# Kernel tuning notes

Measured on AMD Instinct MI355X. Metric: run time of the kernel, lower is better.

## Reference

```python
import jax, jax.numpy as jnp
import numpy as np

B, T, D, MP = 32, 256, 512, 20


def setup_inputs() -> dict:
    key = jax.random.key(0)
    k1, k2, k3 = jax.random.split(key, 3)
    reps_lt = jax.random.normal(k1, (B, T, D), dtype=jnp.float32)
    reps_rt = jax.random.normal(k2, (B, T, D), dtype=jnp.float32)
    kernel = jax.random.normal(k3, (1, 1, 1, MP, D), dtype=jnp.float32)
    return {"reps_lt": reps_lt, "reps_rt": reps_rt, "kernel": kernel}


def reference(reps_lt, reps_rt, kernel):
    # kernel: (1,1,1,m,d) -> (m,d)
    km = kernel.reshape(kernel.shape[-2], kernel.shape[-1])
    # scores[b,t,s,m] = sum_d lt[b,t,d] * km[m,d] * rt[b,s,d]
    # matches original broadcast-multiply + sum over d (cosine_norm=False path)
    scores = jnp.einsum('btd,md,bsd->btsm', reps_lt, km, reps_rt)
    match = jnp.tanh(scores)               # [b, t1, t2, m]
    return jnp.max(match, axis=2)          # max-pool over t2 -> [b, t1, m]
```

## Files before the change

### kernel.cpp

```cpp
#include <hip/hip_runtime.h>


constexpr int TT = 256;
constexpr int DD = 512;
constexpr int NM = 20;
constexpr int NB = 32;
constexpr int BM = 128;
constexpr int BK = 32;
constexpr int NK = DD / BK;

typedef short bf16x8 __attribute__((ext_vector_type(8)));
typedef float f32x4  __attribute__((ext_vector_type(4)));

__device__ __forceinline__ void async_ld16(const void* g, void* l) {
    __builtin_amdgcn_global_load_lds(
        (const __attribute__((address_space(1))) void*)g,
        (__attribute__((address_space(3))) void*)l, 16, 0, 0);
}

__device__ __forceinline__ unsigned pack_bf16(float lo, float hi) {
    unsigned ulo = __builtin_bit_cast(unsigned, lo);
    unsigned uhi = __builtin_bit_cast(unsigned, hi);
    return (ulo >> 16) | (uhi & 0xFFFF0000u);
}

__device__ __forceinline__ unsigned mulpack(unsigned a2, float k0, float k1) {
    float f0 = __builtin_bit_cast(float, a2 << 16) * k0;
    float f1 = __builtin_bit_cast(float, a2 & 0xFFFF0000u) * k1;
    return __builtin_amdgcn_perm(__builtin_bit_cast(unsigned, f1),
                                 __builtin_bit_cast(unsigned, f0), 0x07060302u);
}

__global__ __launch_bounds__(256)
void cast_bf16(const float* __restrict__ lt, const float* __restrict__ rt,
               unsigned short* __restrict__ ltb, unsigned short* __restrict__ rtb)
{
    const int half = (int)gridDim.x >> 1;
    int bid = blockIdx.x;
    const float* src;
    unsigned short* dst;
    if (bid < half) { src = lt; dst = ltb; }
    else            { src = rt; dst = rtb; bid -= half; }
    size_t base = ((size_t)bid * 256 + threadIdx.x) * 8;
    float4 a = *(const float4*)(src + base);
    float4 b = *(const float4*)(src + base + 4);
    uint4 w;
    w.x = pack_bf16(a.x, a.y);
    w.y = pack_bf16(a.z, a.w);
    w.z = pack_bf16(b.x, b.y);
    w.w = pack_bf16(b.z, b.w);
    *(uint4*)(dst + base) = w;
}

__global__ __launch_bounds__(256, 4)
void mp_match_split(const unsigned short* __restrict__ ltb, const unsigned short* __restrict__ rtb,
                    const float* __restrict__ km, float* __restrict__ part)
{
    __shared__ __attribute__((aligned(16))) unsigned short Ash[2][BM * 4 * 8];
    __shared__ __attribute__((aligned(16))) unsigned short Bsh[2][BM * 4 * 8];
    __shared__ __attribute__((aligned(16))) float kmf[DD];
    __shared__ __attribute__((aligned(16))) float maxbuf[2][BM];

    const int f  = blockIdx.x;
    const int c8 = f & 7;
    const int i  = f >> 3;
    const int b  = c8 + 8 * (i / 80);
    const int j  = i % 80;
    const int m  = j >> 2;
    const int t0 = ((j >> 1) & 1) * 128;
    const int s0 = (j & 1) * 128;
    const int sT = j & 1;

    const int tid  = threadIdx.x;
    const int w    = tid >> 6;
    const int lane = tid & 63;
    const int l15  = lane & 15;
    const int l4   = lane >> 4;
    const int wt   = (w & 1) * 64;
    const int wsO  = (w >> 1) * 64;

    kmf[tid]       = km[(size_t)m * DD + tid];
    kmf[tid + 256] = km[(size_t)m * DD + tid + 256];

    const unsigned short* ltB = ltb + ((size_t)b * TT + t0) * DD;
    const unsigned short* rtB = rtb + ((size_t)b * TT + s0) * DD;

    const int ar0 = tid >> 2,        ac = tid & 3;
    const int ar1 = (tid + 256) >> 2;
    const int ap0 = ac ^ ((ar0 >> 1) & 3);
    const int ap1 = ac ^ ((ar1 >> 1) & 3);
    const unsigned short* aSrc0 = ltB + (size_t)ar0 * DD + ac * 8;
    const unsigned short* aSrc1 = ltB + (size_t)ar1 * DD + ac * 8;

    auto issueB = [&](int kk, int buf) {
        const int kb = kk * BK;
#pragma unroll
        for (int q = 0; q < 2; ++q) {
            int slot = q * 256 + tid;
            int row = slot >> 2;
            int c = (slot & 3) ^ ((slot >> 3) & 3);
            async_ld16(rtB + (size_t)row * DD + kb + c * 8,
                       (char*)&Bsh[buf][0] + (size_t)slot * 16);
        }
    };
    auto aload = [&](int kk, uint4* ar) {
        ar[0] = *(const uint4*)(aSrc0 + kk * BK);
        ar[1] = *(const uint4*)(aSrc1 + kk * BK);
    };
    auto scaleWrite = [&](int kk, int buf, const uint4* ar) {
        float4 k0 = *(const float4*)&kmf[kk * BK + ac * 8];
        float4 k1 = *(const float4*)&kmf[kk * BK + ac * 8 + 4];
        uint4 o;
        o.x = mulpack(ar[0].x, k0.x, k0.y);
        o.y = mulpack(ar[0].y, k0.z, k0.w);
        o.z = mulpack(ar[0].z, k1.x, k1.y);
        o.w = mulpack(ar[0].w, k1.z, k1.w);
        *(uint4*)&Ash[buf][(size_t)(ar0 * 4 + ap0) * 8] = o;
        o.x = mulpack(ar[1].x, k0.x, k0.y);
        o.y = mulpack(ar[1].y, k0.z, k0.w);
        o.z = mulpack(ar[1].z, k1.x, k1.y);
        o.w = mulpack(ar[1].w, k1.z, k1.w);
        *(uint4*)&Ash[buf][(size_t)(ar1 * 4 + ap1) * 8] = o;
    };

    f32x4 acc[4][4] = {};
    uint4 ar[2];

    aload(0, ar);
    issueB(0, 0);
    __syncthreads();
    scaleWrite(0, 0, ar);

    const int fpos = l4 ^ ((l15 >> 1) & 3);

    for (int kk = 0; kk < NK; ++kk) {
        const int buf = kk & 1;
        __syncthreads();
        if (kk + 1 < NK) {
            aload(kk + 1, ar);
            issueB(kk + 1, buf ^ 1);
        }
        bf16x8 af[4], bv[4];
#pragma unroll
        for (int ii = 0; ii < 4; ++ii)
            af[ii] = *(const bf16x8*)&Ash[buf][(size_t)((wt + ii * 16 + l15) * 4 + fpos) * 8];
#pragma unroll
        for (int jj = 0; jj < 4; ++jj)
            bv[jj] = *(const bf16x8*)&Bsh[buf][(size_t)((wsO + jj * 16 + l15) * 4 + fpos) * 8];
#pragma unroll
        for (int ii = 0; ii < 4; ++ii)
#pragma unroll
            for (int jj = 0; jj < 4; ++jj)
                acc[ii][jj] = __builtin_amdgcn_mfma_f32_16x16x32_bf16(af[ii], bv[jj], acc[ii][jj], 0, 0, 0);
        if (kk + 1 < NK)
            scaleWrite(kk + 1, buf ^ 1, ar);
    }

#pragma unroll
    for (int ii = 0; ii < 4; ++ii) {
        f32x4 v = acc[ii][0];
#pragma unroll
        for (int jj = 1; jj < 4; ++jj) {
            v.x = fmaxf(v.x, acc[ii][jj].x);
            v.y = fmaxf(v.y, acc[ii][jj].y);
            v.z = fmaxf(v.z, acc[ii][jj].z);
            v.w = fmaxf(v.w, acc[ii][jj].w);
        }
#pragma unroll
        for (int off = 1; off < 16; off <<= 1) {
            v.x = fmaxf(v.x, __shfl_xor(v.x, off, 64));
            v.y = fmaxf(v.y, __shfl_xor(v.y, off, 64));
            v.z = fmaxf(v.z, __shfl_xor(v.z, off, 64));
            v.w = fmaxf(v.w, __shfl_xor(v.w, off, 64));
        }
        if (l15 == 0)
            *(f32x4*)&maxbuf[w >> 1][wt + ii * 16 + l4 * 4] = v;
    }
    __syncthreads();
    if (tid < BM) {
        float v = fmaxf(maxbuf[0][tid], maxbuf[1][tid]);
        part[(((size_t)sT * NB + b) * TT + t0 + tid) * NM + m] = v;
    }
}

__global__ __launch_bounds__(256)
void mp_combine(const float* __restrict__ part, float* __restrict__ out, int n)
{
    int idx = blockIdx.x * 256 + threadIdx.x;
    if (idx < n)
        out[idx] = tanhf(fmaxf(part[idx], part[(size_t)n + idx]));
}

__global__ __launch_bounds__(256, 2)
void mp_match_kernel(const float* __restrict__ lt, const float* __restrict__ rt,
                     const float* __restrict__ km, float* __restrict__ out)
{
    __shared__ __attribute__((aligned(16))) unsigned short Ash[2][4][128][8];
    __shared__ __attribute__((aligned(16))) unsigned short Bsh2[2][4][256][8];
    __shared__ __attribute__((aligned(16))) float maxbuf[2][128];

    const int ttile = blockIdx.x, m = blockIdx.y, b = blockIdx.z;
    const int t0 = ttile * 128;
    const int tid = threadIdx.x, wave = tid >> 6, lane = tid & 63;
    const int l15 = lane & 15, l4 = lane >> 4;
    const int wt = (wave & 1) * 64, wsi = wave >> 1;

    const float* ltp = lt + ((size_t)b * TT + t0) * DD;
    const float* rtp = rt + (size_t)b * TT * DD;
    const float* kmp = km + (size_t)m * DD;
    const int a_t = tid >> 1, a_h = tid & 1;

    f32x4 acc[4][8] = {};

    auto stage = [&](int kk, int buf) {
        const int d0 = kk * BK;
        const float* ap = ltp + (size_t)a_t * DD + d0 + a_h * 16;
        const float* kp = kmp + d0 + a_h * 16;
#pragma unroll
        for (int q = 0; q < 2; ++q) {
            float4 x0 = *(const float4*)(ap + q * 8);
            float4 x1 = *(const float4*)(ap + q * 8 + 4);
            float4 k0 = *(const float4*)(kp + q * 8);
            float4 k1 = *(const float4*)(kp + q * 8 + 4);
            uint4 wv;
            wv.x = pack_bf16(x0.x * k0.x, x0.y * k0.y);
            wv.y = pack_bf16(x0.z * k0.z, x0.w * k0.w);
            wv.z = pack_bf16(x1.x * k1.x, x1.y * k1.y);
            wv.w = pack_bf16(x1.z * k1.z, x1.w * k1.w);
            *(uint4*)&Ash[buf][a_h * 2 + q][a_t][0] = wv;
        }
        const float* bp = rtp + (size_t)tid * DD + d0;
#pragma unroll
        for (int p = 0; p < 4; ++p) {
            float4 y0 = *(const float4*)(bp + p * 8);
            float4 y1 = *(const float4*)(bp + p * 8 + 4);
            uint4 wv;
            wv.x = pack_bf16(y0.x, y0.y);
            wv.y = pack_bf16(y0.z, y0.w);
            wv.z = pack_bf16(y1.x, y1.y);
            wv.w = pack_bf16(y1.z, y1.w);
            *(uint4*)&Bsh2[buf][p][tid][0] = wv;
        }
    };

    stage(0, 0);
    for (int kk = 0; kk < NK; ++kk) {
        const int buf = kk & 1;
        __syncthreads();
        bf16x8 af[4], bfv[8];
#pragma unroll
        for (int i = 0; i < 4; ++i)
            af[i] = *(const bf16x8*)&Ash[buf][l4][wt + i * 16 + l15][0];
#pragma unroll
        for (int j = 0; j < 8; ++j)
            bfv[j] = *(const bf16x8*)&Bsh2[buf][l4][wsi * 128 + j * 16 + l15][0];
        if (kk + 1 < NK) stage(kk + 1, buf ^ 1);
#pragma unroll
        for (int i = 0; i < 4; ++i)
#pragma unroll
            for (int j = 0; j < 8; ++j)
                acc[i][j] = __builtin_amdgcn_mfma_f32_16x16x32_bf16(af[i], bfv[j], acc[i][j], 0, 0, 0);
    }
#pragma unroll
    for (int i = 0; i < 4; ++i) {
        f32x4 v = acc[i][0];
#pragma unroll
        for (int j = 1; j < 8; ++j) {
            v.x = fmaxf(v.x, acc[i][j].x); v.y = fmaxf(v.y, acc[i][j].y);
            v.z = fmaxf(v.z, acc[i][j].z); v.w = fmaxf(v.w, acc[i][j].w);
        }
#pragma unroll
        for (int off = 1; off < 16; off <<= 1) {
            v.x = fmaxf(v.x, __shfl_xor(v.x, off, 64));
            v.y = fmaxf(v.y, __shfl_xor(v.y, off, 64));
            v.z = fmaxf(v.z, __shfl_xor(v.z, off, 64));
            v.w = fmaxf(v.w, __shfl_xor(v.w, off, 64));
        }
        if (l15 == 0) *(f32x4*)&maxbuf[wsi][wt + i * 16 + l4 * 4] = v;
    }
    __syncthreads();
    if (tid < 128) {
        float v = fmaxf(maxbuf[0][tid], maxbuf[1][tid]);
        out[((size_t)b * TT + t0 + tid) * NM + m] = tanhf(v);
    }
}

extern "C" void kernel_launch(void* const* d_in, const int* in_sizes, int n_in,
                              void* d_out, int out_size, void* d_ws, size_t ws_size,
                              hipStream_t stream) {
    const float* lt  = (const float*)d_in[0];
    const float* rt  = (const float*)d_in[1];
    const float* km  = (const float*)d_in[2];
    float*       out = (float*)d_out;

    const size_t elems = (size_t)NB * TT * DD;
    const size_t castB = 2 * elems * sizeof(unsigned short);
    const int    nOut  = NB * TT * NM;
    const size_t partB = 2 * (size_t)nOut * sizeof(float);

    if (ws_size >= castB + partB) {
        unsigned short* ltb = (unsigned short*)d_ws;
        unsigned short* rtb = ltb + elems;
        float* part = (float*)((char*)d_ws + castB);
        cast_bf16<<<4096, 256, 0, stream>>>(lt, rt, ltb, rtb);
        mp_match_split<<<2560, 256, 0, stream>>>(ltb, rtb, km, part);
        mp_combine<<<(nOut + 255) / 256, 256, 0, stream>>>(part, out, nOut);
    } else {
        mp_match_kernel<<<dim3(2, NM, NB), 256, 0, stream>>>(lt, rt, km, out);
    }
}
```

Measured before the change: 133.9 us.

## Switch split matcher to FP8 MFMA with fp32 lt read directly and BK 64

Replaces the bf16 pipeline with FP8. rt is pre-cast to fp8 in a swizzled layout, while lt is read as fp32 inside the match kernel, scaled by the kernel row and packed to fp8 in LDS. This drops the separate lt cast pass and halves the bytes moved through LDS, and it doubles BK to 64 so there are fewer K iterations and barriers. In exchange, fp8 e4m3 precision is much coarser and may break the accuracy tolerance, and per-block global traffic for lt grows because it is now read as fp32.

Result: slower. 139.6 us (+4.2%).

```diff
diff --git a/kernel.cpp b/kernel.cpp
--- a/kernel.cpp
+++ b/kernel.cpp
@@ -6,11 +6,11 @@
 constexpr int NM = 20;
 constexpr int NB = 32;
 constexpr int BM = 128;
-constexpr int BK = 32;
+constexpr int BK = 64;
 constexpr int NK = DD / BK;
 
-typedef short bf16x8 __attribute__((ext_vector_type(8)));
 typedef float f32x4  __attribute__((ext_vector_type(4)));
+typedef long  i64x2  __attribute__((ext_vector_type(2)));
 
 __device__ __forceinline__ void async_ld16(const void* g, void* l) {
     __builtin_amdgcn_global_load_lds(
@@ -24,41 +24,34 @@
     return (ulo >> 16) | (uhi & 0xFFFF0000u);
 }
 
-__device__ __forceinline__ unsigned mulpack(unsigned a2, float k0, float k1) {
-    float f0 = __builtin_bit_cast(float, a2 << 16) * k0;
-    float f1 = __builtin_bit_cast(float, a2 & 0xFFFF0000u) * k1;
-    return __builtin_amdgcn_perm(__builtin_bit_cast(unsigned, f1),
-                                 __builtin_bit_cast(unsigned, f0), 0x07060302u);
+__device__ __forceinline__ unsigned pk4_fp8(float a, float b, float c, float d) {
+    unsigned r = __builtin_amdgcn_cvt_pk_fp8_f32(a, b, 0, false);
+    return __builtin_amdgcn_cvt_pk_fp8_f32(c, d, r, true);
 }
 
 __global__ __launch_bounds__(256)
-void cast_bf16(const float* __restrict__ lt, const float* __restrict__ rt,
-               unsigned short* __restrict__ ltb, unsigned short* __restrict__ rtb)
+void cast_rt_fp8(const float* __restrict__ rt, unsigned char* __restrict__ rtf)
 {
-    const int half = (int)gridDim.x >> 1;
-    int bid = blockIdx.x;
-    const float* src;
-    unsigned short* dst;
-    if (bid < half) { src = lt; dst = ltb; }
-    else            { src = rt; dst = rtb; bid -= half; }
-    size_t base = ((size_t)bid * 256 + threadIdx.x) * 8;
-    float4 a = *(const float4*)(src + base);
-    float4 b = *(const float4*)(src + base + 4);
-    uint4 w;
-    w.x = pack_bf16(a.x, a.y);
-    w.y = pack_bf16(a.z, a.w);
-    w.z = pack_bf16(b.x, b.y);
-    w.w = pack_bf16(b.z, b.w);
-    *(uint4*)(dst + base) = w;
-}
-
-__global__ __launch_bounds__(256, 4)
-void mp_match_split(const unsigned short* __restrict__ ltb, const unsigned short* __restrict__ rtb,
-                    const float* __restrict__ km, float* __restrict__ part)
+    int t   = blockIdx.x * 256 + threadIdx.x;
+    int row = t >> 6;
+    int g6  = t & 63;
+    int kb  = g6 >> 3, q = g6 & 7;
+    int src = ((q & 1) << 5) + ((q >> 1) << 3);
+    const float* p = rt + (size_t)row * DD + kb * 64 + src;
+    float4 a = *(const float4*)p;
+    float4 b = *(const float4*)(p + 4);
+    uint2 o;
+    o.x = pk4_fp8(a.x, a.y, a.z, a.w);
+    o.y = pk4_fp8(b.x, b.y, b.z, b.w);
+    *(uint2*)(rtf + (size_t)row * DD + kb * 64 + q * 8) = o;
+}
+
+__global__ __launch_bounds__(256, 3)
+void mp_match_fp8(const float* __restrict__ lt, const unsigned char* __restrict__ rtf,
+                  const float* __restrict__ km, float* __restrict__ part)
 {
-    __shared__ __attribute__((aligned(16))) unsigned short Ash[2][BM * 4 * 8];
-    __shared__ __attribute__((aligned(16))) unsigned short Bsh[2][BM * 4 * 8];
-    __shared__ __attribute__((aligned(16))) float kmf[DD];
+    __shared__ __attribute__((aligned(16))) unsigned char Ash[2][BM * 64];
+    __shared__ __attribute__((aligned(16))) unsigned char Bsh[2][BM * 64];
     __shared__ __attribute__((aligned(16))) float maxbuf[2][BM];
 
     const int f  = blockIdx.x;
@@ -79,56 +72,56 @@
     const int wt   = (w & 1) * 64;
     const int wsO  = (w >> 1) * 64;
 
-    kmf[tid]       = km[(size_t)m * DD + tid];
-    kmf[tid + 256] = km[(size_t)m * DD + tid + 256];
-
-    const unsigned short* ltB = ltb + ((size_t)b * TT + t0) * DD;
-    const unsigned short* rtB = rtb + ((size_t)b * TT + s0) * DD;
-
-    const int ar0 = tid >> 2,        ac = tid & 3;
-    const int ar1 = (tid + 256) >> 2;
-    const int ap0 = ac ^ ((ar0 >> 1) & 3);
-    const int ap1 = ac ^ ((ar1 >> 1) & 3);
-    const unsigned short* aSrc0 = ltB + (size_t)ar0 * DD + ac * 8;
-    const unsigned short* aSrc1 = ltB + (size_t)ar1 * DD + ac * 8;
+    const float*         ltB = lt  + ((size_t)b * TT + t0) * DD;
+    const unsigned char* rtB = rtf + ((size_t)b * TT + s0) * DD;
+    const float*         kmp = km  + (size_t)m * DD;
+
+    const int arow = tid >> 2, apos = tid & 3;
+    const int ag   = apos ^ ((arow >> 1) & 3);
+    const float* aSrc0 = ltB + (size_t)arow * DD + ag * 8;
+    const float* aSrc1 = aSrc0 + (size_t)64 * DD;
+    const float* kSrc  = kmp + ag * 8;
 
     auto issueB = [&](int kk, int buf) {
-        const int kb = kk * BK;
 #pragma unroll
         for (int q = 0; q < 2; ++q) {
             int slot = q * 256 + tid;
-            int row = slot >> 2;
-            int c = (slot & 3) ^ ((slot >> 3) & 3);
-            async_ld16(rtB + (size_t)row * DD + kb + c * 8,
+            int row  = slot >> 2;
+            int c    = (slot & 3) ^ ((slot >> 3) & 3);
+            async_ld16(rtB + (size_t)row * DD + kk * 64 + c * 16,
                        (char*)&Bsh[buf][0] + (size_t)slot * 16);
         }
     };
-    auto aload = [&](int kk, uint4* ar) {
-        ar[0] = *(const uint4*)(aSrc0 + kk * BK);
-        ar[1] = *(const uint4*)(aSrc1 + kk * BK);
+    auto aload = [&](int kk, float4* ar) {
+        const float* p0 = aSrc0 + kk * 64;
+        const float* p1 = aSrc1 + kk * 64;
+        ar[0] = *(const float4*)p0;        ar[1] = *(const float4*)(p0 + 4);
+        ar[2] = *(const float4*)(p0 + 32); ar[3] = *(const float4*)(p0 + 36);
+        ar[4] = *(const float4*)p1;        ar[5] = *(const float4*)(p1 + 4);
+        ar[6] = *(const float4*)(p1 + 32); ar[7] = *(const float4*)(p1 + 36);
     };
-    auto scaleWrite = [&](int kk, int buf, const uint4* ar) {
-        float4 k0 = *(const float4*)&kmf[kk * BK + ac * 8];
-        float4 k1 = *(const float4*)&kmf[kk * BK + ac * 8 + 4];
+    auto scaleWrite = [&](int kk, int buf, const float4* ar) {
+        const float* kp = kSrc + kk * 64;
+        float4 k0 = *(const float4*)kp;        float4 k1 = *(const float4*)(kp + 4);
+        float4 k2 = *(const float4*)(kp + 32); float4 k3 = *(const float4*)(kp + 36);
         uint4 o;
-        o.x = mulpack(ar[0].x, k0.x, k0.y);
-        o.y = mulpack(ar[0].y, k0.z, k0.w);
-        o.z = mulpack(ar[0].z, k1.x, k1.y);
-        o.w = mulpack(ar[0].w, k1.z, k1.w);
-        *(uint4*)&Ash[buf][(size_t)(ar0 * 4 + ap0) * 8] = o;
-        o.x = mulpack(ar[1].x, k0.x, k0.y);
-        o.y = mulpack(ar[1].y, k0.z, k0.w);
-        o.z = mulpack(ar[1].z, k1.x, k1.y);
-        o.w = mulpack(ar[1].w, k1.z, k1.w);
-        *(uint4*)&Ash[buf][(size_t)(ar1 * 4 + ap1) * 8] = o;
+        o.x = pk4_fp8(ar[0].x*k0.x, ar[0].y*k0.y, ar[0].z*k0.z, ar[0].w*k0.w);
+        o.y = pk4_fp8(ar[1].x*k1.x, ar[1].y*k1.y, ar[1].z*k1.z, ar[1].w*k1.w);
+        o.z = pk4_fp8(ar[2].x*k2.x, ar[2].y*k2.y, ar[2].z*k2.z, ar[2].w*k2.w);
+        o.w = pk4_fp8(ar[3].x*k3.x, ar[3].y*k3.y, ar[3].z*k3.z, ar[3].w*k3.w);
+        *(uint4*)&Ash[buf][(size_t)(arow * 4 + apos) * 16] = o;
+        o.x = pk4_fp8(ar[4].x*k0.x, ar[4].y*k0.y, ar[4].z*k0.z, ar[4].w*k0.w);
+        o.y = pk4_fp8(ar[5].x*k1.x, ar[5].y*k1.y, ar[5].z*k1.z, ar[5].w*k1.w);
+        o.z = pk4_fp8(ar[6].x*k2.x, ar[6].y*k2.y, ar[6].z*k2.z, ar[6].w*k2.w);
+        o.w = pk4_fp8(ar[7].x*k3.x, ar[7].y*k3.y, ar[7].z*k3.z, ar[7].w*k3.w);
+        *(uint4*)&Ash[buf][(size_t)((arow + 64) * 4 + apos) * 16] = o;
     };
 
     f32x4 acc[4][4] = {};
-    uint4 ar[2];
+    float4 ar[8];
 
     aload(0, ar);
     issueB(0, 0);
-    __syncthreads();
     scaleWrite(0, 0, ar);
 
     const int fpos = l4 ^ ((l15 >> 1) & 3);
@@ -140,18 +133,28 @@
             aload(kk + 1, ar);
             issueB(kk + 1, buf ^ 1);
         }
-        bf16x8 af[4], bv[4];
+        uint4 au[4], bu[4];
 #pragma unroll
         for (int ii = 0; ii < 4; ++ii)
-            af[ii] = *(const bf16x8*)&Ash[buf][(size_t)((wt + ii * 16 + l15) * 4 + fpos) * 8];
+            au[ii] = *(const uint4*)&Ash[buf][(size_t)((wt + ii * 16 + l15) * 4 + fpos) * 16];
 #pragma unroll
         for (int jj = 0; jj < 4; ++jj)
-            bv[jj] = *(const bf16x8*)&Bsh[buf][(size_t)((wsO + jj * 16 + l15) * 4 + fpos) * 8];
+            bu[jj] = *(const uint4*)&Bsh[buf][(size_t)((wsO + jj * 16 + l15) * 4 + fpos) * 16];
+        i64x2 a2[4], b2[4];
+#pragma unroll
+        for (int ii = 0; ii < 4; ++ii) a2[ii] = __builtin_bit_cast(i64x2, au[ii]);
+#pragma unroll
+        for (int jj = 0; jj < 4; ++jj) b2[jj] = __builtin_bit_cast(i64x2, bu[jj]);
 #pragma unroll
         for (int ii = 0; ii < 4; ++ii)
 #pragma unroll
             for (int jj = 0; jj < 4; ++jj)
-                acc[ii][jj] = __builtin_amdgcn_mfma_f32_16x16x32_bf16(af[ii], bv[jj], acc[ii][jj], 0, 0, 0);
+                acc[ii][jj] = __builtin_amdgcn_mfma_f32_16x16x32_fp8_fp8(a2[ii].x, b2[jj].x, acc[ii][jj], 0, 0, 0);
+#pragma unroll
+        for (int ii = 0; ii < 4; ++ii)
+#pragma unroll
+            for (int jj = 0; jj < 4; ++jj)
+                acc[ii][jj] = __builtin_amdgcn_mfma_f32_16x16x32_fp8_fp8(a2[ii].y, b2[jj].y, acc[ii][jj], 0, 0, 0);
         if (kk + 1 < NK)
             scaleWrite(kk + 1, buf ^ 1, ar);
     }
@@ -190,6 +193,8 @@
     if (idx < n)
         out[idx] = tanhf(fmaxf(part[idx], part[(size_t)n + idx]));
 }
+
+typedef short bf16x8 __attribute__((ext_vector_type(8)));
 
 __global__ __launch_bounds__(256, 2)
 void mp_match_kernel(const float* __restrict__ lt, const float* __restrict__ rt,
@@ -213,7 +218,7 @@
     f32x4 acc[4][8] = {};
 
     auto stage = [&](int kk, int buf) {
-        const int d0 = kk * BK;
+        const int d0 = kk * 32;
         const float* ap = ltp + (size_t)a_t * DD + d0 + a_h * 16;
         const float* kp = kmp + d0 + a_h * 16;
 #pragma unroll
@@ -244,7 +249,7 @@
     };
 
     stage(0, 0);
-    for (int kk = 0; kk < NK; ++kk) {
+    for (int kk = 0; kk < 16; ++kk) {
         const int buf = kk & 1;
         __syncthreads();
         bf16x8 af[4], bfv[8];
@@ -254,7 +259,7 @@
 #pragma unroll
         for (int j = 0; j < 8; ++j)
             bfv[j] = *(const bf16x8*)&Bsh2[buf][l4][wsi * 128 + j * 16 + l15][0];
-        if (kk + 1 < NK) stage(kk + 1, buf ^ 1);
+        if (kk + 1 < 16) stage(kk + 1, buf ^ 1);
 #pragma unroll
         for (int i = 0; i < 4; ++i)
 #pragma unroll
@@ -294,16 +299,15 @@
     float*       out = (float*)d_out;
 
     const size_t elems = (size_t)NB * TT * DD;
-    const size_t castB = 2 * elems * sizeof(unsigned short);
+    const size_t rtfB  = elems;
     const int    nOut  = NB * TT * NM;
     const size_t partB = 2 * (size_t)nOut * sizeof(float);
 
-    if (ws_size >= castB + partB) {
-        unsigned short* ltb = (unsigned short*)d_ws;
-        unsigned short* rtb = ltb + elems;
-        float* part = (float*)((char*)d_ws + castB);
-        cast_bf16<<<4096, 256, 0, stream>>>(lt, rt, ltb, rtb);
-        mp_match_split<<<2560, 256, 0, stream>>>(ltb, rtb, km, part);
+    if (ws_size >= rtfB + partB) {
+        unsigned char* rtf = (unsigned char*)d_ws;
+        float* part = (float*)((char*)d_ws + rtfB);
+        cast_rt_fp8<<<(int)(elems / 8 / 256), 256, 0, stream>>>(rt, rtf);
+        mp_match_fp8<<<2560, 256, 0, stream>>>(lt, rtf, km, part);
         mp_combine<<<(nOut + 255) / 256, 256, 0, stream>>>(part, out, nOut);
     } else {
         mp_match_kernel<<<dim3(2, NM, NB), 256, 0, stream>>>(lt, rt, km, out);
```
